# Kernel tuning notes

Measured on AMD Instinct MI355X. Metric: run time of the kernel, lower is better.

The kernel has to match this reference:

```python
import jax, jax.numpy as jnp
import numpy as np

EPS = 1e-12  # matches torch F.normalize eps clamp


def _l2norm(v, axis):
    n = jnp.sqrt(jnp.sum(v * v, axis=axis, keepdims=True))
    return v / jnp.maximum(n, EPS)


def setup_inputs() -> dict:
    key = jax.random.key(0)
    k1, k2, k3, k4 = jax.random.split(key, 4)
    N, C, H, W, K = 64, 128, 64, 64, 64
    x = jax.random.normal(k1, (N, C, H, W), dtype=jnp.float32)
    conv_w = jax.random.normal(k2, (K, C), dtype=jnp.float32) * 0.1  # 1x1 conv weight squeezed
    conv_b = jax.random.normal(k3, (K,), dtype=jnp.float32) * 0.1
    centroids = jax.random.uniform(k4, (K, C), dtype=jnp.float32)
    return {"x": x, "conv_w": conv_w, "conv_b": conv_b, "centroids": centroids}


def reference(x, conv_w, conv_b, centroids):
    N, C = x.shape[:2]
    K = centroids.shape[0]
    xf = x.reshape(N, C, -1)                                   # (N, C, P) with P = H*W
    # 1x1 conv == per-pixel linear map over channels
    logits = jnp.einsum('ncp,kc->nkp', xf, conv_w) + conv_b[None, :, None]
    a = jax.nn.softmax(logits, axis=1)                         # soft assignment over clusters
    # vlad[n,k,c] = sum_p a[n,k,p] * (x[n,c,p] - centroids[k,c])
    vlad = jnp.einsum('nkp,ncp->nkc', a, xf) \
        - jnp.sum(a, axis=-1)[:, :, None] * centroids[None]    # (N, K, C)
    vlad = _l2norm(vlad, axis=2)                               # intra-cluster normalization
    vlad = vlad.reshape(N, K * C)
    return _l2norm(vlad, axis=1)
```

## Files before the change

### kernel.cpp

```cpp
#include <hip/hip_runtime.h>
#include <math.h>

#define NNIMG 64
#define CCH 128
#define KK 64
#define PP 4096
#define BSPLIT 8
#define PB (PP / BSPLIT)
#define PC 64
#define NCHUNK (PB / PC)

typedef __attribute__((ext_vector_type(8))) short short8;
typedef __attribute__((ext_vector_type(4))) float f32x4;

__device__ inline unsigned short bf16_hi(float f) {
  unsigned u = __float_as_uint(f);
  unsigned r = u + 0x7FFFu + ((u >> 16) & 1u);
  return (unsigned short)(r >> 16);
}
__device__ inline float bf16_tof(unsigned short h) {
  return __uint_as_float(((unsigned)h) << 16);
}

__global__ __launch_bounds__(256, 2) void netvlad_main(
    const float* __restrict__ x, const float* __restrict__ conv_w,
    const float* __restrict__ conv_b, float* __restrict__ vlad_part,
    float* __restrict__ asum_part) {
  __shared__ unsigned int pc_hl[PC * 132];
  __shared__ unsigned short cp_hi[CCH * 72];
  __shared__ unsigned short a_lds[KK * 72];
  __shared__ float b_lds[KK];
  __shared__ float asum_buf[4 * KK];

  const int t = threadIdx.x;
  const int lane = t & 63;
  const int w = t >> 6;
  const int m = lane & 15;
  const int q = lane >> 4;

  const int n = blockIdx.x / BSPLIT;
  const int blk = blockIdx.x % BSPLIT;

  if (t < KK) b_lds[t] = conv_b[t];

  short8 Whi[4][4], Wlo[4][4];
#pragma unroll
  for (int kt = 0; kt < 4; ++kt) {
#pragma unroll
    for (int cs = 0; cs < 4; ++cs) {
      const float* wp = conv_w + (kt * 16 + m) * CCH + cs * 32 + q * 8;
      float4 wa = *(const float4*)wp;
      float4 wb = *(const float4*)(wp + 4);
      float fv[8] = {wa.x, wa.y, wa.z, wa.w, wb.x, wb.y, wb.z, wb.w};
      short8 h, l;
#pragma unroll
      for (int j = 0; j < 8; ++j) {
        unsigned short hb = bf16_hi(fv[j]);
        h[j] = (short)hb;
        l[j] = (short)bf16_hi(fv[j] - bf16_tof(hb));
      }
      Whi[kt][cs] = h;
      Wlo[kt][cs] = l;
    }
  }

  f32x4 vacc[4][2];
#pragma unroll
  for (int kt = 0; kt < 4; ++kt)
#pragma unroll
    for (int ct = 0; ct < 2; ++ct) vacc[kt][ct] = (f32x4){0.f, 0.f, 0.f, 0.f};
  float asum_acc[16];
#pragma unroll
  for (int i = 0; i < 16; ++i) asum_acc[i] = 0.f;

  const int crow = t >> 3;
  const int pr = t & 7;
  const int prow_w = w * 16 + m;
  const int swz_r = 8 * ((prow_w >> 2) & 3);

#pragma unroll 1
  for (int ch = 0; ch < NCHUNK; ++ch) {
    __syncthreads();
    const float* xb = x + (size_t)n * CCH * PP + blk * PB + ch * PC;
#pragma unroll
    for (int ci = 0; ci < 4; ++ci) {
      int c = crow + ci * 32;
      const float* xr = xb + (size_t)c * PP;
#pragma unroll
      for (int rep = 0; rep < 2; ++rep) {
        int pl = pr * 4 + rep * 32;
        float4 v = *(const float4*)(xr + pl);
        float fv[4] = {v.x, v.y, v.z, v.w};
        unsigned short h[4], lo[4];
#pragma unroll
        for (int j = 0; j < 4; ++j) {
          h[j] = bf16_hi(fv[j]);
          lo[j] = bf16_hi(fv[j] - bf16_tof(h[j]));
        }
        uint2 cpv;
        cpv.x = (unsigned)h[0] | ((unsigned)h[1] << 16);
        cpv.y = (unsigned)h[2] | ((unsigned)h[3] << 16);
        *(uint2*)&cp_hi[c * 72 + pl] = cpv;
        int cc = c ^ (8 * ((pl >> 2) & 3));
#pragma unroll
        for (int j = 0; j < 4; ++j)
          pc_hl[(pl + j) * 132 + cc] = (unsigned)h[j] | ((unsigned)lo[j] << 16);
      }
    }
    __syncthreads();

    f32x4 acc1[4];
#pragma unroll
    for (int kt = 0; kt < 4; ++kt) acc1[kt] = (f32x4){0.f, 0.f, 0.f, 0.f};
    const unsigned int* pcrow = pc_hl + prow_w * 132;
#pragma unroll
    for (int cs = 0; cs < 4; ++cs) {
      int base = cs * 32 + ((q << 3) ^ swz_r);
      uint4 s0 = *(const uint4*)&pcrow[base];
      uint4 s1 = *(const uint4*)&pcrow[base + 4];
      unsigned int ss[8] = {s0.x, s0.y, s0.z, s0.w, s1.x, s1.y, s1.z, s1.w};
      unsigned int hs[4], ls[4];
#pragma unroll
      for (int i = 0; i < 4; ++i) {
        hs[i] = __builtin_amdgcn_perm(ss[2 * i + 1], ss[2 * i], 0x05040100u);
        ls[i] = __builtin_amdgcn_perm(ss[2 * i + 1], ss[2 * i], 0x07060302u);
      }
      short8 Bh, Bl;
      __builtin_memcpy(&Bh, hs, 16);
      __builtin_memcpy(&Bl, ls, 16);
#pragma unroll
      for (int kt = 0; kt < 4; ++kt) {
        acc1[kt] = __builtin_amdgcn_mfma_f32_16x16x32_bf16(Whi[kt][cs], Bh, acc1[kt], 0, 0, 0);
        acc1[kt] = __builtin_amdgcn_mfma_f32_16x16x32_bf16(Whi[kt][cs], Bl, acc1[kt], 0, 0, 0);
        acc1[kt] = __builtin_amdgcn_mfma_f32_16x16x32_bf16(Wlo[kt][cs], Bh, acc1[kt], 0, 0, 0);
      }
    }

    float ssum = 0.f;
#pragma unroll
    for (int kt = 0; kt < 4; ++kt)
#pragma unroll
      for (int r = 0; r < 4; ++r) {
        float e = __expf(acc1[kt][r] + b_lds[kt * 16 + q * 4 + r]);
        acc1[kt][r] = e;
        ssum += e;
      }
    ssum += __shfl_xor(ssum, 16, 64);
    ssum += __shfl_xor(ssum, 32, 64);
    float inv = 1.0f / ssum;
#pragma unroll
    for (int kt = 0; kt < 4; ++kt)
#pragma unroll
      for (int r = 0; r < 4; ++r) {
        float a = acc1[kt][r] * inv;
        asum_acc[kt * 4 + r] += a;
        a_lds[(kt * 16 + q * 4 + r) * 72 + prow_w] = bf16_hi(a);
      }
    __syncthreads();

#pragma unroll
    for (int ps = 0; ps < 2; ++ps) {
      short8 Af[4];
#pragma unroll
      for (int kt = 0; kt < 4; ++kt)
        Af[kt] = *(const short8*)&a_lds[(kt * 16 + m) * 72 + ps * 32 + q * 8];
#pragma unroll
      for (int ct = 0; ct < 2; ++ct) {
        short8 Bf = *(const short8*)&cp_hi[(w * 32 + ct * 16 + m) * 72 + ps * 32 + q * 8];
#pragma unroll
        for (int kt = 0; kt < 4; ++kt)
          vacc[kt][ct] = __builtin_amdgcn_mfma_f32_16x16x32_bf16(Af[kt], Bf, vacc[kt][ct], 0, 0, 0);
      }
    }
  }

  const size_t vbase = (size_t)blockIdx.x * (KK * CCH);
#pragma unroll
  for (int kt = 0; kt < 4; ++kt)
#pragma unroll
    for (int ct = 0; ct < 2; ++ct)
#pragma unroll
      for (int r = 0; r < 4; ++r)
        vlad_part[vbase + (kt * 16 + q * 4 + r) * CCH + (w * 32 + ct * 16 + m)] =
            vacc[kt][ct][r];
#pragma unroll
  for (int i = 0; i < 16; ++i) {
    float v = asum_acc[i];
    v += __shfl_xor(v, 1, 64);
    v += __shfl_xor(v, 2, 64);
    v += __shfl_xor(v, 4, 64);
    v += __shfl_xor(v, 8, 64);
    if (m == 0) asum_buf[w * 64 + (i >> 2) * 16 + q * 4 + (i & 3)] = v;
  }
  __syncthreads();
  if (t < 64) {
    float s = asum_buf[t] + asum_buf[64 + t] + asum_buf[128 + t] + asum_buf[192 + t];
    asum_part[blockIdx.x * 64 + t] = s;
  }
}

__global__ __launch_bounds__(256) void netvlad_finish(
    const float* __restrict__ vlad_part, const float* __restrict__ asum_part,
    const float* __restrict__ centroids, float* __restrict__ out) {
  const int t = threadIdx.x;
  const int w = t >> 6, ln = t & 63;
  const int idx = blockIdx.x * 4 + w;
  const int n = idx >> 6, k = idx & 63;
  const int c = ln * 2;
  float v0 = 0.f, v1 = 0.f;
#pragma unroll
  for (int b = 0; b < BSPLIT; ++b) {
    float2 pv = *(const float2*)&vlad_part[(size_t)(n * BSPLIT + b) * (KK * CCH) + k * CCH + c];
    v0 += pv.x;
    v1 += pv.y;
  }
  float s = 0.f;
#pragma unroll
  for (int b = 0; b < BSPLIT; ++b) s += asum_part[(n * BSPLIT + b) * KK + k];
  float2 ce = *(const float2*)&centroids[k * CCH + c];
  v0 -= s * ce.x;
  v1 -= s * ce.y;
  float ssq = v0 * v0 + v1 * v1;
#pragma unroll
  for (int off = 32; off > 0; off >>= 1) ssq += __shfl_xor(ssq, off, 64);
  float inv = 0.125f / fmaxf(sqrtf(ssq), 1e-12f);
  float2 o;
  o.x = v0 * inv;
  o.y = v1 * inv;
  *(float2*)&out[(size_t)n * (KK * CCH) + k * CCH + c] = o;
}

extern "C" void kernel_launch(void* const* d_in, const int* in_sizes, int n_in,
                              void* d_out, int out_size, void* d_ws, size_t ws_size,
                              hipStream_t stream) {
  const float* x = (const float*)d_in[0];
  const float* conv_w = (const float*)d_in[1];
  const float* conv_b = (const float*)d_in[2];
  const float* centroids = (const float*)d_in[3];
  float* out = (float*)d_out;

  float* vlad_part = (float*)d_ws;
  float* asum_part = vlad_part + (size_t)NNIMG * BSPLIT * KK * CCH;

  netvlad_main<<<NNIMG * BSPLIT, 256, 0, stream>>>(x, conv_w, conv_b, vlad_part, asum_part);
  netvlad_finish<<<NNIMG * KK / 4, 256, 0, stream>>>(vlad_part, asum_part, centroids, out);
}
```

Measured before the change: 246.9 us.

## Register-prefetch next x chunk, drop cp_hi LDS copy, stage output via LDS

The main loop is restructured into a double-buffered body that issues the global loads for the next chunk into registers before converting and storing the current one, so memory latency overlaps compute. The separate cp_hi bf16 LDS buffer is removed. The second GEMM's B operand is instead gathered from the packed pc_hl tile with scalar LDS reads and byte permutes, which cuts LDS footprint and store traffic. __syncthreads is replaced by an explicit lgkmcnt wait plus s_barrier. The final partial-VLAD write is staged through LDS so global stores become coalesced float4. The cost is more registers for the prefetch buffers and more scalar LDS reads for the gathered B fragments.

Measured after the change: 275.6 us. +11.6%, slower.

```diff
diff --git a/kernel.cpp b/kernel.cpp
--- a/kernel.cpp
+++ b/kernel.cpp
@@ -13,13 +13,24 @@
 typedef __attribute__((ext_vector_type(8))) short short8;
 typedef __attribute__((ext_vector_type(4))) float f32x4;
 
-__device__ inline unsigned short bf16_hi(float f) {
+__device__ __forceinline__ unsigned short bf16_hi(float f) {
   unsigned u = __float_as_uint(f);
   unsigned r = u + 0x7FFFu + ((u >> 16) & 1u);
   return (unsigned short)(r >> 16);
 }
-__device__ inline float bf16_tof(unsigned short h) {
+__device__ __forceinline__ float bf16_tof(unsigned short h) {
   return __uint_as_float(((unsigned)h) << 16);
+}
+__device__ __forceinline__ unsigned pack_hl(float f) {
+  unsigned u = __float_as_uint(f);
+  unsigned r = u + 0x7FFFu + ((u >> 16) & 1u);
+  float hf = __uint_as_float(r & 0xFFFF0000u);
+  unsigned lo = __float_as_uint(f - hf);
+  return __builtin_amdgcn_perm(lo, r, 0x07060302u);
+}
+
+__device__ __forceinline__ void lgkm_barrier() {
+  __asm__ volatile("s_waitcnt lgkmcnt(0)\n\ts_barrier" ::: "memory");
 }
 
 __global__ __launch_bounds__(256, 2) void netvlad_main(
@@ -27,14 +38,13 @@
     const float* __restrict__ conv_b, float* __restrict__ vlad_part,
     float* __restrict__ asum_part) {
   __shared__ unsigned int pc_hl[PC * 132];
-  __shared__ unsigned short cp_hi[CCH * 72];
   __shared__ unsigned short a_lds[KK * 72];
   __shared__ float b_lds[KK];
   __shared__ float asum_buf[4 * KK];
 
   const int t = threadIdx.x;
   const int lane = t & 63;
-  const int w = t >> 6;
+  const int wv = t >> 6;
   const int m = lane & 15;
   const int q = lane >> 4;
 
@@ -75,44 +85,36 @@
 
   const int crow = t >> 3;
   const int pr = t & 7;
-  const int prow_w = w * 16 + m;
-  const int swz_r = 8 * ((prow_w >> 2) & 3);
-
-#pragma unroll 1
-  for (int ch = 0; ch < NCHUNK; ++ch) {
-    __syncthreads();
-    const float* xb = x + (size_t)n * CCH * PP + blk * PB + ch * PC;
+  const int prow = wv * 16 + m;
+  const int swz_r = 8 * ((prow >> 2) & 3);
+  const float* xbase = x + (size_t)n * CCH * PP + blk * PB;
+
+  auto body = [&](float4 (&cur)[8], float4 (&nxt)[8], const float* nb) {
+#pragma unroll
+    for (int ci = 0; ci < 4; ++ci)
+#pragma unroll
+      for (int rep = 0; rep < 2; ++rep)
+        nxt[ci * 2 + rep] =
+            *(const float4*)(nb + (size_t)(crow + ci * 32) * PP + pr * 4 + rep * 32);
+
 #pragma unroll
     for (int ci = 0; ci < 4; ++ci) {
-      int c = crow + ci * 32;
-      const float* xr = xb + (size_t)c * PP;
+      int cc = (crow + ci * 32) ^ (8 * (pr & 3));
 #pragma unroll
       for (int rep = 0; rep < 2; ++rep) {
         int pl = pr * 4 + rep * 32;
-        float4 v = *(const float4*)(xr + pl);
+        float4 v = cur[ci * 2 + rep];
         float fv[4] = {v.x, v.y, v.z, v.w};
-        unsigned short h[4], lo[4];
-#pragma unroll
-        for (int j = 0; j < 4; ++j) {
-          h[j] = bf16_hi(fv[j]);
-          lo[j] = bf16_hi(fv[j] - bf16_tof(h[j]));
-        }
-        uint2 cpv;
-        cpv.x = (unsigned)h[0] | ((unsigned)h[1] << 16);
-        cpv.y = (unsigned)h[2] | ((unsigned)h[3] << 16);
-        *(uint2*)&cp_hi[c * 72 + pl] = cpv;
-        int cc = c ^ (8 * ((pl >> 2) & 3));
-#pragma unroll
-        for (int j = 0; j < 4; ++j)
-          pc_hl[(pl + j) * 132 + cc] = (unsigned)h[j] | ((unsigned)lo[j] << 16);
-      }
-    }
-    __syncthreads();
+#pragma unroll
+        for (int j = 0; j < 4; ++j) pc_hl[(pl + j) * 132 + cc] = pack_hl(fv[j]);
+      }
+    }
+    lgkm_barrier();
 
     f32x4 acc1[4];
 #pragma unroll
     for (int kt = 0; kt < 4; ++kt) acc1[kt] = (f32x4){0.f, 0.f, 0.f, 0.f};
-    const unsigned int* pcrow = pc_hl + prow_w * 132;
+    const unsigned int* pcrow = pc_hl + prow * 132;
 #pragma unroll
     for (int cs = 0; cs < 4; ++cs) {
       int base = cs * 32 + ((q << 3) ^ swz_r);
@@ -136,6 +138,23 @@
       }
     }
 
+    unsigned int bg[4][4];
+#pragma unroll
+    for (int ct = 0; ct < 2; ++ct)
+#pragma unroll
+      for (int ps = 0; ps < 2; ++ps) {
+        int c = wv * 32 + ct * 16 + m;
+        unsigned int g[8];
+#pragma unroll
+        for (int j = 0; j < 8; ++j) {
+          int p = ps * 32 + q * 8 + j;
+          g[j] = pc_hl[p * 132 + (c ^ (8 * ((p >> 2) & 3)))];
+        }
+#pragma unroll
+        for (int i = 0; i < 4; ++i)
+          bg[ct * 2 + ps][i] = __builtin_amdgcn_perm(g[2 * i + 1], g[2 * i], 0x05040100u);
+      }
+
     float ssum = 0.f;
 #pragma unroll
     for (int kt = 0; kt < 4; ++kt)
@@ -154,9 +173,9 @@
       for (int r = 0; r < 4; ++r) {
         float a = acc1[kt][r] * inv;
         asum_acc[kt * 4 + r] += a;
-        a_lds[(kt * 16 + q * 4 + r) * 72 + prow_w] = bf16_hi(a);
-      }
-    __syncthreads();
+        a_lds[(kt * 16 + q * 4 + r) * 72 + prow] = bf16_hi(a);
+      }
+    lgkm_barrier();
 
 #pragma unroll
     for (int ps = 0; ps < 2; ++ps) {
@@ -166,23 +185,37 @@
         Af[kt] = *(const short8*)&a_lds[(kt * 16 + m) * 72 + ps * 32 + q * 8];
 #pragma unroll
       for (int ct = 0; ct < 2; ++ct) {
-        short8 Bf = *(const short8*)&cp_hi[(w * 32 + ct * 16 + m) * 72 + ps * 32 + q * 8];
+        short8 Bf;
+        __builtin_memcpy(&Bf, bg[ct * 2 + ps], 16);
 #pragma unroll
         for (int kt = 0; kt < 4; ++kt)
           vacc[kt][ct] = __builtin_amdgcn_mfma_f32_16x16x32_bf16(Af[kt], Bf, vacc[kt][ct], 0, 0, 0);
       }
     }
-  }
-
-  const size_t vbase = (size_t)blockIdx.x * (KK * CCH);
+  };
+
+  float4 bufA[8], bufB[8];
+#pragma unroll
+  for (int ci = 0; ci < 4; ++ci)
+#pragma unroll
+    for (int rep = 0; rep < 2; ++rep)
+      bufA[ci * 2 + rep] =
+          *(const float4*)(xbase + (size_t)(crow + ci * 32) * PP + pr * 4 + rep * 32);
+
+#pragma unroll 1
+  for (int ch = 0; ch < NCHUNK; ch += 2) {
+    body(bufA, bufB, xbase + (ch + 1) * PC);
+    body(bufB, bufA, xbase + ((ch + 2) & (NCHUNK - 1)) * PC);
+  }
+
+  float* vt = (float*)pc_hl;
 #pragma unroll
   for (int kt = 0; kt < 4; ++kt)
 #pragma unroll
     for (int ct = 0; ct < 2; ++ct)
 #pragma unroll
       for (int r = 0; r < 4; ++r)
-        vlad_part[vbase + (kt * 16 + q * 4 + r) * CCH + (w * 32 + ct * 16 + m)] =
-            vacc[kt][ct][r];
+        vt[(kt * 16 + q * 4 + r) * 132 + wv * 32 + ct * 16 + m] = vacc[kt][ct][r];
 #pragma unroll
   for (int i = 0; i < 16; ++i) {
     float v = asum_acc[i];
@@ -190,9 +223,16 @@
     v += __shfl_xor(v, 2, 64);
     v += __shfl_xor(v, 4, 64);
     v += __shfl_xor(v, 8, 64);
-    if (m == 0) asum_buf[w * 64 + (i >> 2) * 16 + q * 4 + (i & 3)] = v;
-  }
-  __syncthreads();
+    if (m == 0) asum_buf[wv * 64 + (i >> 2) * 16 + q * 4 + (i & 3)] = v;
+  }
+  lgkm_barrier();
+  {
+    const int k = t >> 2, c0 = (t & 3) * 32;
+    const size_t ob = (size_t)blockIdx.x * (KK * CCH) + k * CCH + c0;
+#pragma unroll
+    for (int i = 0; i < 8; ++i)
+      *(float4*)&vlad_part[ob + i * 4] = *(const float4*)&vt[k * 132 + c0 + i * 4];
+  }
   if (t < 64) {
     float s = asum_buf[t] + asum_buf[64 + t] + asum_buf[128 + t] + asum_buf[192 + t];
     asum_part[blockIdx.x * 64 + t] = s;
```
